# Performance work log

Hardware: AMD Instinct MI355X
Metric: run time of the kernel (lower is better)

## Reference

```python
import jax, jax.numpy as jnp
import numpy as np

INPUT_DIM = 1024
NUM_TARGETS = 128
BATCH = 32768


def setup_inputs() -> dict:
    key = jax.random.key(0)
    kx, kw, kb = jax.random.split(key, 3)
    x = jax.random.normal(kx, (BATCH, INPUT_DIM), dtype=jnp.float32)
    # Fused view of num_targets independent nn.Linear(input_dim, 1) layers:
    # column t of W / entry t of b are the weights/bias of layer t.
    bound = 1.0 / np.sqrt(INPUT_DIM)  # torch Linear default init range
    W = jax.random.uniform(kw, (INPUT_DIM, NUM_TARGETS), minval=-bound, maxval=bound, dtype=jnp.float32)
    b = jax.random.uniform(kb, (NUM_TARGETS,), minval=-bound, maxval=bound, dtype=jnp.float32)
    return {"x": x, "W": W, "b": b}


def reference(x, W, b):
    # Equivalent to concatenating sigmoid(Linear_t(x)) over t along last dim:
    # one fused matmul [B,D]x[D,T] + bias + sigmoid.
    return jax.nn.sigmoid(x @ W + b)
```

## Files before the change

kernel.cpp:

```cpp
#include <hip/hip_runtime.h>
#include <hip/hip_bf16.h>


typedef __bf16 bf16x8 __attribute__((ext_vector_type(8)));
typedef float  f32x4  __attribute__((ext_vector_type(4)));

#define DIM   1024
#define NT    128
#define BATCH 32768

__global__ __launch_bounds__(256) void prep_w(const float* __restrict__ W,
                                              __bf16* __restrict__ wsW) {
    int idx = blockIdx.x * 256 + threadIdx.x;
    int j = idx & 7;
    int l = (idx >> 3) & 63;
    int c = (idx >> 9) & 7;
    int s = idx >> 12;
    int k = s * 32 + (l >> 4) * 8 + j;
    int n = c * 16 + (l & 15);
    wsW[idx] = (__bf16)W[k * NT + n];
}

__device__ __forceinline__ bf16x8 cvt_bf16x8(float4 a0, float4 a1) {
    bf16x8 af;
    af[0] = (__bf16)a0.x; af[1] = (__bf16)a0.y;
    af[2] = (__bf16)a0.z; af[3] = (__bf16)a0.w;
    af[4] = (__bf16)a1.x; af[5] = (__bf16)a1.y;
    af[6] = (__bf16)a1.z; af[7] = (__bf16)a1.w;
    return af;
}

__global__ __launch_bounds__(256, 2) void gemm_bias_sigmoid(
        const float* __restrict__ x,
        const __hip_bfloat16* __restrict__ wsWh,
        const float* __restrict__ bias,
        float* __restrict__ out) {
    const bf16x8* __restrict__ wsW8 = (const bf16x8*)wsWh;

    const int tid  = threadIdx.x;
    const int lane = tid & 63;
    const int wave = tid >> 6;
    const int q    = lane >> 4;
    const int r    = lane & 15;
    const int row0 = blockIdx.x * 64 + wave * 16;

    const float*  xA  = x + (size_t)(row0 + r) * DIM + q * 8;
    const bf16x8* gB  = wsW8 + lane;

    f32x4 acc[8];
#pragma unroll
    for (int c = 0; c < 8; ++c)
        acc[c] = (f32x4){0.f, 0.f, 0.f, 0.f};

#pragma unroll
    for (int s = 0; s < 32; ++s) {
        const float* ap = xA + (size_t)s * 32;
        const float4 a0 = *(const float4*)ap;
        const float4 a1 = *(const float4*)(ap + 4);
        const bf16x8 af = cvt_bf16x8(a0, a1);
#pragma unroll
        for (int c = 0; c < 8; ++c) {
            const bf16x8 bf = gB[(s * 8 + c) * 64];
            acc[c] = __builtin_amdgcn_mfma_f32_16x16x32_bf16(af, bf, acc[c], 0, 0, 0);
        }
    }

#pragma unroll
    for (int c = 0; c < 8; ++c) {
        const float bv = bias[c * 16 + r];
#pragma unroll
        for (int reg = 0; reg < 4; ++reg) {
            const int row = row0 + q * 4 + reg;
            float v = acc[c][reg] + bv;
            v = 1.0f / (1.0f + __expf(-v));
            out[(size_t)row * NT + c * 16 + r] = v;
        }
    }
}

extern "C" void kernel_launch(void* const* d_in, const int* in_sizes, int n_in,
                              void* d_out, int out_size, void* d_ws, size_t ws_size,
                              hipStream_t stream) {
    const float* x = (const float*)d_in[0];
    const float* W = (const float*)d_in[1];
    const float* b = (const float*)d_in[2];
    float* out     = (float*)d_out;
    __bf16* wsW    = (__bf16*)d_ws;

    prep_w<<<DIM * NT / 256, 256, 0, stream>>>(W, wsW);
    gemm_bias_sigmoid<<<BATCH / 64, 256, 0, stream>>>(
        x, (const __hip_bfloat16*)wsW, b, out);
}
```

Baseline: 248.8 us.

## Stage W slice in LDS, split output columns across blocks, prefetch x

```diff
diff --git a/kernel.cpp b/kernel.cpp
--- a/kernel.cpp
+++ b/kernel.cpp
@@ -30,50 +30,78 @@
     return af;
 }
 
-__global__ __launch_bounds__(256, 2) void gemm_bias_sigmoid(
+__global__ __launch_bounds__(512, 4) void gemm_bias_sigmoid(
         const float* __restrict__ x,
         const __hip_bfloat16* __restrict__ wsWh,
         const float* __restrict__ bias,
         float* __restrict__ out) {
     const bf16x8* __restrict__ wsW8 = (const bf16x8*)wsWh;
+    __shared__ bf16x8 ldsW[4096];
 
     const int tid  = threadIdx.x;
     const int lane = tid & 63;
     const int wave = tid >> 6;
     const int q    = lane >> 4;
     const int r    = lane & 15;
-    const int row0 = blockIdx.x * 64 + wave * 16;
 
-    const float*  xA  = x + (size_t)(row0 + r) * DIM + q * 8;
-    const bf16x8* gB  = wsW8 + lane;
+    const int u    = blockIdx.x;
+    const int xcd  = u & 7;
+    const int jj   = u >> 3;
+    const int t    = xcd * 32 + (jj >> 2);
+    const int h    = jj & 3;
+    const int wrow = t * 128 + wave * 16;
 
-    f32x4 acc[8];
+    const float* xA = x + (size_t)(wrow + r) * DIM + q * 8;
+
+#define LOADA(B, S)                                                    \
+    {                                                                  \
+        const float* ap_ = xA + (size_t)(S) * 32;                      \
+        Aa[B] = *(const float4*)ap_;                                   \
+        Ab[B] = *(const float4*)(ap_ + 4);                             \
+    }
+
+    float4 Aa[3], Ab[3];
+    LOADA(0, 0)
+    LOADA(1, 1)
+    LOADA(2, 2)
+
 #pragma unroll
-    for (int c = 0; c < 8; ++c)
-        acc[c] = (f32x4){0.f, 0.f, 0.f, 0.f};
+    for (int i = 0; i < 8; ++i) {
+        const int m  = wave * 8 + i;
+        const int s  = m >> 1;
+        const int cp = m & 1;
+        const bf16x8* gsrc = wsW8 + (size_t)(s * 8 + h * 2 + cp) * 64 + lane;
+        __builtin_amdgcn_global_load_lds(
+            (const __attribute__((address_space(1))) void*)gsrc,
+            (__attribute__((address_space(3))) void*)&ldsW[m * 64],
+            16, 0, 0);
+    }
+    __syncthreads();
+
+    f32x4 acc[2];
+    acc[0] = (f32x4){0.f, 0.f, 0.f, 0.f};
+    acc[1] = (f32x4){0.f, 0.f, 0.f, 0.f};
 
 #pragma unroll
     for (int s = 0; s < 32; ++s) {
-        const float* ap = xA + (size_t)s * 32;
-        const float4 a0 = *(const float4*)ap;
-        const float4 a1 = *(const float4*)(ap + 4);
-        const bf16x8 af = cvt_bf16x8(a0, a1);
-#pragma unroll
-        for (int c = 0; c < 8; ++c) {
-            const bf16x8 bf = gB[(s * 8 + c) * 64];
-            acc[c] = __builtin_amdgcn_mfma_f32_16x16x32_bf16(af, bf, acc[c], 0, 0, 0);
-        }
+        const int b = s % 3;
+        const bf16x8 af = cvt_bf16x8(Aa[b], Ab[b]);
+        if (s + 3 < 32) LOADA(b, s + 3)
+        const bf16x8* bp = &ldsW[s * 128 + lane];
+        acc[0] = __builtin_amdgcn_mfma_f32_16x16x32_bf16(af, bp[0],  acc[0], 0, 0, 0);
+        acc[1] = __builtin_amdgcn_mfma_f32_16x16x32_bf16(af, bp[64], acc[1], 0, 0, 0);
     }
+#undef LOADA
 
 #pragma unroll
-    for (int c = 0; c < 8; ++c) {
-        const float bv = bias[c * 16 + r];
+    for (int c = 0; c < 2; ++c) {
+        const float bv = bias[h * 32 + c * 16 + r];
 #pragma unroll
         for (int reg = 0; reg < 4; ++reg) {
-            const int row = row0 + q * 4 + reg;
+            const int row = wrow + q * 4 + reg;
             float v = acc[c][reg] + bv;
             v = 1.0f / (1.0f + __expf(-v));
-            out[(size_t)row * NT + c * 16 + r] = v;
+            out[(size_t)row * NT + h * 32 + c * 16 + r] = v;
         }
     }
 }
@@ -88,6 +116,6 @@
     __bf16* wsW    = (__bf16*)d_ws;
 
     prep_w<<<DIM * NT / 256, 256, 0, stream>>>(W, wsW);
-    gemm_bias_sigmoid<<<BATCH / 64, 256, 0, stream>>>(
+    gemm_bias_sigmoid<<<BATCH / 32, 512, 0, stream>>>(
         x, (const __hip_bfloat16*)wsW, b, out);
 }
```

New measurement: 229.5 us. 7.8% less time.

## Software-pipeline A and B global loads with triple buffering and explicit vmcnt waits

Applied to the files above, without the earlier changes.

```diff
diff --git a/kernel.cpp b/kernel.cpp
--- a/kernel.cpp
+++ b/kernel.cpp
@@ -30,6 +30,40 @@
     return af;
 }
 
+#define WVM2(n) asm volatile("s_waitcnt vmcnt(" #n ")" ::: "memory")
+#define WVM(n)  do { WVM2(n); __builtin_amdgcn_sched_barrier(0); } while (0)
+
+template<int BK, int S>
+__device__ __forceinline__ void issueB(bf16x8 (&Bb)[3][8], const bf16x8* gB) {
+#pragma unroll
+    for (int c = 0; c < 8; ++c)
+        asm volatile("global_load_dwordx4 %0, %1, off"
+                     : "=v"(Bb[BK][c]) : "v"(gB + (S * 8 + c) * 64));
+}
+
+template<int BK, int S>
+__device__ __forceinline__ void issueA(float4 (&Aa)[3], float4 (&Ab)[3],
+                                       const float* xA) {
+    asm volatile("global_load_dwordx4 %0, %1, off"
+                 : "=v"(Aa[BK]) : "v"(xA + S * 32));
+    asm volatile("global_load_dwordx4 %0, %1, off"
+                 : "=v"(Ab[BK]) : "v"(xA + S * 32 + 4));
+}
+
+template<int BK>
+__device__ __forceinline__ bf16x8 cvtA(float4 (&Aa)[3], float4 (&Ab)[3]) {
+    return cvt_bf16x8(Aa[BK], Ab[BK]);
+}
+
+template<int BK>
+__device__ __forceinline__ void mfma8(bf16x8 af, bf16x8 (&Bb)[3][8],
+                                      f32x4 (&acc)[8]) {
+#pragma unroll
+    for (int c = 0; c < 8; ++c)
+        acc[c] = __builtin_amdgcn_mfma_f32_16x16x32_bf16(af, Bb[BK][c],
+                                                         acc[c], 0, 0, 0);
+}
+
 __global__ __launch_bounds__(256, 2) void gemm_bias_sigmoid(
         const float* __restrict__ x,
         const __hip_bfloat16* __restrict__ wsWh,
@@ -44,26 +78,68 @@
     const int r    = lane & 15;
     const int row0 = blockIdx.x * 64 + wave * 16;
 
-    const float*  xA  = x + (size_t)(row0 + r) * DIM + q * 8;
-    const bf16x8* gB  = wsW8 + lane;
+    const float*  xA = x + (size_t)(row0 + r) * DIM + q * 8;
+    const bf16x8* gB = wsW8 + lane;
 
     f32x4 acc[8];
 #pragma unroll
     for (int c = 0; c < 8; ++c)
         acc[c] = (f32x4){0.f, 0.f, 0.f, 0.f};
 
-#pragma unroll
-    for (int s = 0; s < 32; ++s) {
-        const float* ap = xA + (size_t)s * 32;
-        const float4 a0 = *(const float4*)ap;
-        const float4 a1 = *(const float4*)(ap + 4);
-        const bf16x8 af = cvt_bf16x8(a0, a1);
-#pragma unroll
-        for (int c = 0; c < 8; ++c) {
-            const bf16x8 bf = gB[(s * 8 + c) * 64];
-            acc[c] = __builtin_amdgcn_mfma_f32_16x16x32_bf16(af, bf, acc[c], 0, 0, 0);
-        }
-    }
+    float4 Aa[3], Ab[3];
+    bf16x8 Bb[3][8];
+
+    issueA<0, 0>(Aa, Ab, xA);
+    issueA<1, 1>(Aa, Ab, xA);
+    issueA<2, 2>(Aa, Ab, xA);
+    issueB<0, 0>(Bb, gB);
+    issueB<1, 1>(Bb, gB);
+
+#define ST(BN, SB, WN, BA, SA)                                        \
+    { issueB<BN, SB>(Bb, gB); WVM(WN);                                \
+      bf16x8 af = cvtA<BA>(Aa, Ab); issueA<BA, SA>(Aa, Ab, xA);       \
+      mfma8<BA>(af, Bb, acc); }
+#define STNA(BN, SB, WN, BA)                                          \
+    { issueB<BN, SB>(Bb, gB); WVM(WN);                                \
+      bf16x8 af = cvtA<BA>(Aa, Ab); mfma8<BA>(af, Bb, acc); }
+#define STNB(WN, BA)                                                  \
+    { WVM(WN); bf16x8 af = cvtA<BA>(Aa, Ab); mfma8<BA>(af, Bb, acc); }
+
+    ST(2,  2, 16, 0,  3)
+    ST(0,  3, 18, 1,  4)
+    ST(1,  4, 20, 2,  5)
+    ST(2,  5, 20, 0,  6)
+    ST(0,  6, 20, 1,  7)
+    ST(1,  7, 20, 2,  8)
+    ST(2,  8, 20, 0,  9)
+    ST(0,  9, 20, 1, 10)
+    ST(1, 10, 20, 2, 11)
+    ST(2, 11, 20, 0, 12)
+    ST(0, 12, 20, 1, 13)
+    ST(1, 13, 20, 2, 14)
+    ST(2, 14, 20, 0, 15)
+    ST(0, 15, 20, 1, 16)
+    ST(1, 16, 20, 2, 17)
+    ST(2, 17, 20, 0, 18)
+    ST(0, 18, 20, 1, 19)
+    ST(1, 19, 20, 2, 20)
+    ST(2, 20, 20, 0, 21)
+    ST(0, 21, 20, 1, 22)
+    ST(1, 22, 20, 2, 23)
+    ST(2, 23, 20, 0, 24)
+    ST(0, 24, 20, 1, 25)
+    ST(1, 25, 20, 2, 26)
+    ST(2, 26, 20, 0, 27)
+    ST(0, 27, 20, 1, 28)
+    ST(1, 28, 20, 2, 29)
+    ST(2, 29, 20, 0, 30)
+    ST(0, 30, 20, 1, 31)
+    STNA(1, 31, 20, 2)
+    STNB(10, 0)
+    STNB(0, 1)
+#undef ST
+#undef STNA
+#undef STNB
 
 #pragma unroll
     for (int c = 0; c < 8; ++c) {
```

New measurement: 213.0 us. -14.4%, faster.

## Stage bf16 weights through LDS with async loads and triple-buffer x rows

Applied to the files above, without the earlier changes.

```diff
diff --git a/kernel.cpp b/kernel.cpp
--- a/kernel.cpp
+++ b/kernel.cpp
@@ -30,40 +30,89 @@
     return af;
 }
 
-__global__ __launch_bounds__(256, 2) void gemm_bias_sigmoid(
+__global__ __launch_bounds__(512, 4) void gemm_bias_sigmoid(
         const float* __restrict__ x,
         const __hip_bfloat16* __restrict__ wsWh,
         const float* __restrict__ bias,
         float* __restrict__ out) {
     const bf16x8* __restrict__ wsW8 = (const bf16x8*)wsWh;
+    __shared__ bf16x8 ldsW[4096];
 
     const int tid  = threadIdx.x;
     const int lane = tid & 63;
     const int wave = tid >> 6;
     const int q    = lane >> 4;
     const int r    = lane & 15;
-    const int row0 = blockIdx.x * 64 + wave * 16;
+    const int row0 = blockIdx.x * 128 + wave * 16;
 
-    const float*  xA  = x + (size_t)(row0 + r) * DIM + q * 8;
-    const bf16x8* gB  = wsW8 + lane;
+    const float* xA = x + (size_t)(row0 + r) * DIM + q * 8;
 
     f32x4 acc[8];
 #pragma unroll
     for (int c = 0; c < 8; ++c)
         acc[c] = (f32x4){0.f, 0.f, 0.f, 0.f};
 
-#pragma unroll
-    for (int s = 0; s < 32; ++s) {
-        const float* ap = xA + (size_t)s * 32;
-        const float4 a0 = *(const float4*)ap;
-        const float4 a1 = *(const float4*)(ap + 4);
-        const bf16x8 af = cvt_bf16x8(a0, a1);
-#pragma unroll
-        for (int c = 0; c < 8; ++c) {
-            const bf16x8 bf = gB[(s * 8 + c) * 64];
-            acc[c] = __builtin_amdgcn_mfma_f32_16x16x32_bf16(af, bf, acc[c], 0, 0, 0);
-        }
+    float4 QA[4], QB[4], QC[4];
+
+#define LOADQ(Q, S)                                                     \
+    {                                                                   \
+        const float* ap_ = xA + (size_t)(S) * 32;                       \
+        Q[0] = *(const float4*)ap_;  Q[1] = *(const float4*)(ap_ + 4);  \
+        const float* aq_ = ap_ + 32;                                    \
+        Q[2] = *(const float4*)aq_;  Q[3] = *(const float4*)(aq_ + 4);  \
     }
+
+#define COMP2(Q, SL)                                                        \
+    {                                                                       \
+        const bf16x8 af0 = cvt_bf16x8(Q[0], Q[1]);                          \
+        _Pragma("unroll")                                                   \
+        for (int c = 0; c < 8; ++c)                                         \
+            acc[c] = __builtin_amdgcn_mfma_f32_16x16x32_bf16(               \
+                af0, ldsW[((SL) * 8 + c) * 64 + lane], acc[c], 0, 0, 0);    \
+        const bf16x8 af1 = cvt_bf16x8(Q[2], Q[3]);                          \
+        _Pragma("unroll")                                                   \
+        for (int c = 0; c < 8; ++c)                                         \
+            acc[c] = __builtin_amdgcn_mfma_f32_16x16x32_bf16(               \
+                af1, ldsW[((SL) * 8 + 8 + c) * 64 + lane], acc[c], 0, 0, 0);\
+    }
+
+#define STAGE(P)                                                            \
+    {                                                                       \
+        _Pragma("unroll")                                                   \
+        for (int i = 0; i < 8; ++i) {                                       \
+            const int m = wave * 8 + i;                                     \
+            const bf16x8* gsrc = wsW8 + (size_t)(P) * 4096 + m * 64 + lane; \
+            __builtin_amdgcn_global_load_lds(                               \
+                (const __attribute__((address_space(1))) void*)gsrc,        \
+                (__attribute__((address_space(3))) void*)&ldsW[m * 64],     \
+                16, 0, 0);                                                  \
+        }                                                                   \
+    }
+
+#define PHASE(P, X, Y, Z, LAST)                                             \
+    {                                                                       \
+        __syncthreads();                      \
+        STAGE(P)                                                            \
+        LOADQ(Z, (P) * 8 + 4)            \
+        __syncthreads();                           \
+        COMP2(X, 0) LOADQ(X, (P) * 8 + 6)                                   \
+        COMP2(Y, 2) if (!(LAST)) LOADQ(Y, (P) * 8 + 8)                      \
+        COMP2(Z, 4) if (!(LAST)) LOADQ(Z, (P) * 8 + 10)                     \
+        COMP2(X, 6)                                                         \
+    }
+
+    LOADQ(QA, 0)
+    LOADQ(QB, 2)
+
+    PHASE(0, QA, QB, QC, 0)
+    PHASE(1, QB, QC, QA, 0)
+    PHASE(2, QC, QA, QB, 0)
+    PHASE(3, QA, QB, QC, 1)
+
+#undef PHASE
+#undef STAGE
+#undef COMP2
+#undef LOADQ
 
 #pragma unroll
     for (int c = 0; c < 8; ++c) {
@@ -88,6 +137,6 @@
     __bf16* wsW    = (__bf16*)d_ws;
 
     prep_w<<<DIM * NT / 256, 256, 0, stream>>>(W, wsW);
-    gemm_bias_sigmoid<<<BATCH / 64, 256, 0, stream>>>(
+    gemm_bias_sigmoid<<<BATCH / 128, 512, 0, stream>>>(
         x, (const __hip_bfloat16*)wsW, b, out);
 }
```

Measured after the change: 211.3 us. 15.1% less time.
